# Performance work log

Hardware: AMD Instinct MI355X
Metric: run time of the kernel (lower is better)

Reference implementation:

```python
import jax, jax.numpy as jnp
import numpy as np

B, T, N, F = 64, 512, 14, 16
H_LSTM, H_GCN = 128, 64


def setup_inputs() -> dict:
    key = jax.random.key(0)
    ks = jax.random.split(key, 12)
    s = 0.05
    return {
        "x": jax.random.normal(ks[0], (B, T, N, F), dtype=jnp.float32),
        "adj": jax.random.uniform(ks[1], (N, N), dtype=jnp.float32),
        "W_ih": jax.random.normal(ks[2], (4 * H_LSTM, F), dtype=jnp.float32) * s,
        "W_hh": jax.random.normal(ks[3], (4 * H_LSTM, H_LSTM), dtype=jnp.float32) * s,
        "b_ih": jax.random.normal(ks[4], (4 * H_LSTM,), dtype=jnp.float32) * s,
        "b_hh": jax.random.normal(ks[5], (4 * H_LSTM,), dtype=jnp.float32) * s,
        "W_gcn": jax.random.normal(ks[6], (H_GCN, H_LSTM), dtype=jnp.float32) * s,
        "b_gcn": jax.random.normal(ks[7], (H_GCN,), dtype=jnp.float32) * s,
        "W_out": jax.random.normal(ks[8], (1, H_GCN), dtype=jnp.float32) * s,
        "b_out": jax.random.normal(ks[9], (1,), dtype=jnp.float32) * s,
        "W_lin1": jax.random.normal(ks[10], (28, N), dtype=jnp.float32) * s,
        "b_lin1": jax.random.normal(ks[11], (28,), dtype=jnp.float32) * s,
    }


def _lstm_last(x_seq, W_ih, W_hh, b_ih, b_hh):
    # x_seq: [M, T, F]; single-layer LSTM, torch gate order (i, f, g, o).
    M = x_seq.shape[0]
    H = W_hh.shape[1]
    # Precompute input contribution for all timesteps: [T, M, 4H]
    xw = jnp.einsum('mtf,gf->tmg', x_seq, W_ih) + b_ih + b_hh

    def step(carry, xt):
        h, c = carry
        gates = xt + h @ W_hh.T
        i, f, g, o = jnp.split(gates, 4, axis=-1)
        i = jax.nn.sigmoid(i)
        f = jax.nn.sigmoid(f)
        g = jnp.tanh(g)
        o = jax.nn.sigmoid(o)
        c = f * c + i * g
        h = o * jnp.tanh(c)
        return (h, c), None

    h0 = jnp.zeros((M, H), dtype=x_seq.dtype)
    (h_last, _), _ = jax.lax.scan(step, (h0, h0), xw)
    return h_last  # [M, H]


def reference(x, adj, W_ih, W_hh, b_ih, b_hh, W_gcn, b_gcn, W_out, b_out, W_lin1, b_lin1):
    Bb, Tt, Nn, Ff = x.shape
    # Batch all N node sequences into one recurrent pass (same math as per-node loop).
    x_nodes = x.transpose(0, 2, 1, 3).reshape(Bb * Nn, Tt, Ff)  # [B*N, T, F]
    h_last = _lstm_last(x_nodes, W_ih, W_hh, b_ih, b_hh)        # [B*N, H]
    lstm_out = h_last.reshape(Bb, Nn, -1)                        # [B, N, H]

    # Normalized adjacency with self-loops: D^-1/2 (A+I) D^-1/2
    A_hat = adj + jnp.eye(Nn, dtype=adj.dtype)
    d = A_hat.sum(axis=1) ** -0.5
    A_norm = d[:, None] * A_hat * d[None, :]

    x_gcn = jnp.einsum('ij,bjk->bik', A_norm, lstm_out)          # [B, N, H]
    x_gcn = jax.nn.relu(x_gcn @ W_gcn.T + b_gcn)                 # [B, N, H_GCN]
    x_gcn = (x_gcn @ W_out.T + b_out).squeeze(-1)                # [B, N]
    out = jax.nn.sigmoid(x_gcn @ W_lin1.T + b_lin1)              # [B, 28]
    return out
```

## Files before the change

kernel.cpp:

```cpp
#include <hip/hip_runtime.h>
#include <hip/hip_bf16.h>

#define B_   64
#define T_   512
#define N_   14
#define F_   16
#define H_   128
#define G4_  512
#define TCH  64
#define MBLK 4
#define NBLK 224

typedef __attribute__((ext_vector_type(8))) short bfrag;
typedef __attribute__((ext_vector_type(4))) float facc;
typedef __attribute__((ext_vector_type(4))) int   v4i;

#define L2E   1.4426950408889634f
#define L2E2  2.8853900817779268f

#define SX   0
#define SH   16384
#define LDSZ 17408

__device__ __forceinline__ short f2bf(float f) {
    unsigned u = __builtin_bit_cast(unsigned, f);
    return (short)((u + 0x7FFFu + ((u >> 16) & 1u)) >> 16);
}
__device__ __forceinline__ float bf2f(unsigned short s) {
    return __builtin_bit_cast(float, (unsigned)s << 16);
}
__device__ __forceinline__ unsigned cvt_pk_bf16(float a, float b) {
    unsigned r;
    asm("v_cvt_pk_bf16_f32 %0, %1, %2" : "=v"(r) : "v"(a), "v"(b));
    return r;
}
__device__ __forceinline__ v4i mfma_i8(v4i a, v4i b, v4i c) {
    v4i d;
    asm("v_mfma_i32_16x16x64_i8 %0, %1, %2, %3"
        : "=&v"(d) : "v"(a), "v"(b), "v"(c));
    return d;
}
__device__ __forceinline__ void bar() {
    asm volatile("s_waitcnt lgkmcnt(0)" ::: "memory");
    __builtin_amdgcn_s_barrier();
    asm volatile("" ::: "memory");
}

__global__ void prep1_kernel(const float* __restrict__ W_hh,
                             const float* __restrict__ b_ih, const float* __restrict__ b_hh,
                             float* __restrict__ inv127, float* __restrict__ sw,
                             float* __restrict__ bias) {
    const int g = threadIdx.x;
    float mx = 0.0f;
    for (int k = 0; k < H_; ++k) mx = fmaxf(mx, fabsf(W_hh[g * H_ + k]));
    const float sc = (g >= 256 && g < 384) ? L2E2 : L2E;
    inv127[g] = 127.0f / mx;
    sw[g]     = mx * sc * (1.0f / 16129.0f);
    bias[g]   = (b_ih[g] + b_hh[g]) * sc;
}

__global__ void prep2_kernel(const float* __restrict__ W_hh, const float* __restrict__ W_ih,
                             const float* __restrict__ inv127,
                             signed char* __restrict__ w8, short* __restrict__ wih_bf) {
    const int i = blockIdx.x * blockDim.x + threadIdx.x;
    if (i < G4_ * H_)
        w8[i] = (signed char)(int)rintf(W_hh[i] * inv127[i >> 7]);
    if (i < G4_ * 32) {
        const int n = i >> 5, k = i & 31;
        const float sc = (n >= 256 && n < 384) ? L2E2 : L2E;
        wih_bf[i] = (k < F_) ? f2bf(W_ih[n * F_ + k] * sc) : (short)0;
    }
}

template<int P, bool PREF>
__device__ __forceinline__ void lstm_step(char* lds, int tl,
    const v4i (&B8)[4][2], const bfrag (&Bx)[4], const facc (&bsp)[4],
    const float (&sw4)[4], facc (&xacc)[4], float& cc,
    int hrd, int xrd, int wboff)
{
    bar();
    const char* hb = lds + SH + P * 512;
    const v4i a0 = *(const v4i*)(hb + hrd);
    const v4i a1 = *(const v4i*)(hb + hrd + 256);

    const v4i z4 = (v4i){0, 0, 0, 0};
    v4i acc[4];
#pragma unroll
    for (int q = 0; q < 4; ++q) acc[q] = mfma_i8(a0, B8[q][0], z4);
#pragma unroll
    for (int q = 0; q < 4; ++q) acc[q] = mfma_i8(a1, B8[q][1], acc[q]);

    float z[4];
#pragma unroll
    for (int q = 0; q < 4; ++q)
        z[q] = (float)acc[q][0] * sw4[q] + xacc[q][0];

    const float ea = exp2f(-z[0]);
    const float ef = exp2f(-z[1]);
    const float eo = exp2f(-z[3]);
    const float eg = exp2f(-fabsf(z[2]));
    const float d1 = (1.0f + ea) * (1.0f + eg);
    const float d2 = 1.0f + ef;
    const float rP = __builtin_amdgcn_rcpf(d1 * d2);
    const float ig = __builtin_copysignf((1.0f - eg) * (rP * d2), z[2]);
    cc = (rP * d1) * cc + ig;
    const float ec = exp2f(-L2E2 * fabsf(cc));
    const float hv = __builtin_copysignf(
        (1.0f - ec) * __builtin_amdgcn_rcpf((1.0f + eo) * (1.0f + ec)), cc);
    *(signed char*)(lds + SH + (P ^ 1) * 512 + wboff) =
        (signed char)(int)rintf(hv * 127.0f);

    if (PREF) {
        const bfrag ax = *(const bfrag*)(lds + SX + (tl + 1) * 256 + xrd);
#pragma unroll
        for (int q = 0; q < 4; ++q)
            xacc[q] = __builtin_amdgcn_mfma_f32_16x16x32_bf16(ax, Bx[q], bsp[q], 0, 0, 0);
    }
}

__global__ __launch_bounds__(512, 2) void lstm_kernel(
    const float* __restrict__ x,
    const signed char* __restrict__ w8,
    const short* __restrict__ wih_bf,
    const float* __restrict__ bias,
    const float* __restrict__ sw,
    unsigned short* __restrict__ h_out)
{
    const int m0  = blockIdx.x * MBLK;
    const int tid = threadIdx.x;
    const int w   = tid >> 6, l = tid & 63;
    const int lr  = l & 15, lk = l >> 4;
    const int hcol = w * 16 + lr;

    __shared__ __align__(16) char lds[LDSZ];

    v4i   B8[4][2];
    bfrag Bx[4];
    facc  bsp[4];
    float sw4[4];
#pragma unroll
    for (int q = 0; q < 4; ++q) {
        const int n = q * H_ + hcol;
#pragma unroll
        for (int ks = 0; ks < 2; ++ks)
            B8[q][ks] = *(const v4i*)(w8 + n * 128 + ks * 64 + lk * 16);
        Bx[q] = *(const bfrag*)(wih_bf + n * 32 + lk * 8);
        const float b = bias[n];
        bsp[q] = (facc){b, b, b, b};
        sw4[q] = sw[n];
    }
#pragma unroll
    for (int q = 0; q < 4; ++q) {
        asm volatile("" : "+v"(B8[q][0]));
        asm volatile("" : "+v"(B8[q][1]));
        asm volatile("" : "+v"(Bx[q]));
        asm volatile("" : "+v"(bsp[q]));
    }

    const int hrd = lk * 64 + (lr >> 2) * 16;
    const int xrd = (lr >> 2) * 64 + lk * 16;
    const int wboff = w * 64 + lk * 16 + lr;

    const int skb = tid & 1, sseq = (tid >> 1) & 3, stl = tid >> 3;
    const int seqg = m0 + sseq;
    const int bb = seqg / N_, nn = seqg % N_;
    const float* xq = x + (((size_t)bb * T_ + stl) * N_ + nn) * F_ + skb * 8;
    const int sbyte = SX + stl * 256 + sseq * 64 + skb * 16;

    for (int i = tid; i < LDSZ / 4; i += 512) ((int*)lds)[i] = 0;
    float4 p0 = *(const float4*)xq, p1 = *(const float4*)(xq + 4);

    float cc = 0.0f;
    facc  xacc[4];
    bar();

#pragma unroll 1
    for (int chunk = 0; chunk < T_ / TCH; ++chunk) {
        {
            uint4 o;
            o.x = cvt_pk_bf16(p0.x, p0.y); o.y = cvt_pk_bf16(p0.z, p0.w);
            o.z = cvt_pk_bf16(p1.x, p1.y); o.w = cvt_pk_bf16(p1.z, p1.w);
            *(uint4*)(lds + sbyte) = o;
        }
        if (chunk + 1 < T_ / TCH) {
            xq += TCH * N_ * F_;
            p0 = *(const float4*)xq; p1 = *(const float4*)(xq + 4);
        }
        bar();

        {
            const bfrag ax = *(const bfrag*)(lds + SX + xrd);
#pragma unroll
            for (int q = 0; q < 4; ++q)
                xacc[q] = __builtin_amdgcn_mfma_f32_16x16x32_bf16(ax, Bx[q], bsp[q], 0, 0, 0);
        }

#pragma unroll 1
        for (int tl = 0; tl < TCH; tl += 2) {
            lstm_step<0, true>(lds, tl, B8, Bx, bsp, sw4, xacc, cc,
                               hrd, xrd, wboff);
            if (tl + 2 < TCH)
                lstm_step<1, true>(lds, tl + 1, B8, Bx, bsp, sw4, xacc, cc,
                                   hrd, xrd, wboff);
            else
                lstm_step<1, false>(lds, tl + 1, B8, Bx, bsp, sw4, xacc, cc,
                                    hrd, xrd, wboff);
        }
    }
    bar();

    {
        const int g = tid >> 7, c = tid & 127;
        const int addr = SH + (c >> 4) * 64 + g * 16 + (c & 15);
        const signed char v = *(const signed char*)(lds + addr);
        h_out[(size_t)(m0 + g) * H_ + c] = f2bf((float)v * (1.0f / 127.0f));
    }
}

__global__ __launch_bounds__(256) void head_kernel(
    const float* __restrict__ adj,
    const float* __restrict__ W_gcn, const float* __restrict__ b_gcn,
    const float* __restrict__ W_out, const float* __restrict__ b_out,
    const float* __restrict__ W_lin1, const float* __restrict__ b_lin1,
    const unsigned short* __restrict__ h_in,
    float* __restrict__ out)
{
    const int b   = blockIdx.x;
    const int tid = threadIdx.x;

    __shared__ float s_A[N_][N_];
    __shared__ float s_d[N_];
    __shared__ float s_h[N_][H_];
    __shared__ float s_xg[N_][H_];
    __shared__ float s_g1[N_][64];
    __shared__ float s_s[N_];

    for (int idx = tid; idx < N_ * H_; idx += 256)
        s_h[idx >> 7][idx & 127] = bf2f(h_in[(size_t)b * N_ * H_ + idx]);

    if (tid < N_) {
        float sum = 0.0f;
        for (int j = 0; j < N_; ++j)
            sum += adj[tid * N_ + j] + (tid == j ? 1.0f : 0.0f);
        s_d[tid] = rsqrtf(sum);
    }
    __syncthreads();

    if (tid < N_ * N_) {
        const int i = tid / N_, j = tid % N_;
        const float a = adj[i * N_ + j] + (i == j ? 1.0f : 0.0f);
        s_A[i][j] = s_d[i] * a * s_d[j];
    }
    __syncthreads();

    for (int idx = tid; idx < N_ * H_; idx += 256) {
        const int i = idx >> 7, k = idx & 127;
        float acc = 0.0f;
#pragma unroll
        for (int j = 0; j < N_; ++j) acc += s_A[i][j] * s_h[j][k];
        s_xg[i][k] = acc;
    }
    __syncthreads();

    for (int idx = tid; idx < N_ * 64; idx += 256) {
        const int i = idx >> 6, q = idx & 63;
        float a0 = 0.f, a1 = 0.f, a2 = 0.f, a3 = 0.f;
#pragma unroll
        for (int k = 0; k < H_; k += 4) {
            a0 += s_xg[i][k+0] * W_gcn[q * H_ + k+0];
            a1 += s_xg[i][k+1] * W_gcn[q * H_ + k+1];
            a2 += s_xg[i][k+2] * W_gcn[q * H_ + k+2];
            a3 += s_xg[i][k+3] * W_gcn[q * H_ + k+3];
        }
        const float acc = b_gcn[q] + ((a0 + a1) + (a2 + a3));
        s_g1[i][q] = fmaxf(acc, 0.0f);
    }
    __syncthreads();

    if (tid < N_) {
        float acc = b_out[0];
#pragma unroll
        for (int q = 0; q < 64; ++q) acc += s_g1[tid][q] * W_out[q];
        s_s[tid] = acc;
    }
    __syncthreads();

    if (tid < 28) {
        float acc = b_lin1[tid];
#pragma unroll
        for (int i = 0; i < N_; ++i) acc += s_s[i] * W_lin1[tid * N_ + i];
        out[b * 28 + tid] = 1.0f / (1.0f + __expf(-acc));
    }
}

extern "C" void kernel_launch(void* const* d_in, const int* in_sizes, int n_in,
                              void* d_out, int out_size, void* d_ws, size_t ws_size,
                              hipStream_t stream) {
    const float* x      = (const float*)d_in[0];
    const float* adj    = (const float*)d_in[1];
    const float* W_ih   = (const float*)d_in[2];
    const float* W_hh   = (const float*)d_in[3];
    const float* b_ih   = (const float*)d_in[4];
    const float* b_hh   = (const float*)d_in[5];
    const float* W_gcn  = (const float*)d_in[6];
    const float* b_gcn  = (const float*)d_in[7];
    const float* W_out  = (const float*)d_in[8];
    const float* b_out  = (const float*)d_in[9];
    const float* W_lin1 = (const float*)d_in[10];
    const float* b_lin1 = (const float*)d_in[11];
    float* out = (float*)d_out;

    char* ws = (char*)d_ws;
    signed char*    w8     = (signed char*)(ws);
    short*          wih_bf = (short*)(ws + 65536);
    float*          bias   = (float*)(ws + 98304);
    float*          sw     = (float*)(ws + 100352);
    float*          inv127 = (float*)(ws + 102400);
    unsigned short* h_last = (unsigned short*)(ws + 104448);

    prep1_kernel<<<1, 512, 0, stream>>>(W_hh, b_ih, b_hh, inv127, sw, bias);
    prep2_kernel<<<128, 512, 0, stream>>>(W_hh, W_ih, inv127, w8, wih_bf);
    lstm_kernel<<<NBLK, 512, 0, stream>>>(x, w8, wih_bf, bias, sw, h_last);
    head_kernel<<<B_, 256, 0, stream>>>(adj, W_gcn, b_gcn, W_out, b_out,
                                        W_lin1, b_lin1, h_last, out);
}
```

Measured before the change: 258.5 us.

## Halve sequences per LSTM block and use 4 waves each computing two hidden column tiles

Each LSTM block now handles 2 sequences instead of 4 and launches 448 blocks of 256 threads, so the work spreads across more CUs. Each wave covers 32 hidden columns using two MFMA column tiles, and each lane picks its own column's result (c1 select). Bias is now added in the scalar path instead of being folded into the MFMA accumulator. The cost is twice as many MFMAs per wave per step with half the useful rows, traded for more parallel blocks along the serial time recurrence.

```diff
diff --git a/kernel.cpp b/kernel.cpp
--- a/kernel.cpp
+++ b/kernel.cpp
@@ -8,8 +8,8 @@
 #define H_   128
 #define G4_  512
 #define TCH  64
-#define MBLK 4
-#define NBLK 224
+#define MBLK 2
+#define NBLK 448
 
 typedef __attribute__((ext_vector_type(8))) short bfrag;
 typedef __attribute__((ext_vector_type(4))) float facc;
@@ -19,8 +19,8 @@
 #define L2E2  2.8853900817779268f
 
 #define SX   0
-#define SH   16384
-#define LDSZ 17408
+#define SH   8192
+#define LDSZ 8704
 
 __device__ __forceinline__ short f2bf(float f) {
     unsigned u = __builtin_bit_cast(unsigned, f);
@@ -74,26 +74,36 @@
 
 template<int P, bool PREF>
 __device__ __forceinline__ void lstm_step(char* lds, int tl,
-    const v4i (&B8)[4][2], const bfrag (&Bx)[4], const facc (&bsp)[4],
-    const float (&sw4)[4], facc (&xacc)[4], float& cc,
-    int hrd, int xrd, int wboff)
+    const v4i (&B8)[4][2][2], const bfrag (&Bx)[4][2],
+    const float (&sw_own)[4], const float (&bias_own)[4],
+    facc (&xacc)[4][2], float& cc,
+    int hrd, int xrd, int wboff, bool c1)
 {
     bar();
-    const char* hb = lds + SH + P * 512;
+    const char* hb = lds + SH + P * 256;
     const v4i a0 = *(const v4i*)(hb + hrd);
-    const v4i a1 = *(const v4i*)(hb + hrd + 256);
+    const v4i a1 = *(const v4i*)(hb + hrd + 128);
 
     const v4i z4 = (v4i){0, 0, 0, 0};
-    v4i acc[4];
-#pragma unroll
-    for (int q = 0; q < 4; ++q) acc[q] = mfma_i8(a0, B8[q][0], z4);
-#pragma unroll
-    for (int q = 0; q < 4; ++q) acc[q] = mfma_i8(a1, B8[q][1], acc[q]);
+    v4i acc[4][2];
+#pragma unroll
+    for (int q = 0; q < 4; ++q)
+#pragma unroll
+        for (int c = 0; c < 2; ++c)
+            acc[q][c] = mfma_i8(a0, B8[q][0][c], z4);
+#pragma unroll
+    for (int q = 0; q < 4; ++q)
+#pragma unroll
+        for (int c = 0; c < 2; ++c)
+            acc[q][c] = mfma_i8(a1, B8[q][1][c], acc[q][c]);
 
     float z[4];
 #pragma unroll
-    for (int q = 0; q < 4; ++q)
-        z[q] = (float)acc[q][0] * sw4[q] + xacc[q][0];
+    for (int q = 0; q < 4; ++q) {
+        const int   ia = c1 ? acc[q][1][0] : acc[q][0][0];
+        const float xa = c1 ? xacc[q][1][0] : xacc[q][0][0];
+        z[q] = (float)ia * sw_own[q] + (xa + bias_own[q]);
+    }
 
     const float ea = exp2f(-z[0]);
     const float ef = exp2f(-z[1]);
@@ -107,18 +117,21 @@
     const float ec = exp2f(-L2E2 * fabsf(cc));
     const float hv = __builtin_copysignf(
         (1.0f - ec) * __builtin_amdgcn_rcpf((1.0f + eo) * (1.0f + ec)), cc);
-    *(signed char*)(lds + SH + (P ^ 1) * 512 + wboff) =
+    *(signed char*)(lds + SH + (P ^ 1) * 256 + wboff) =
         (signed char)(int)rintf(hv * 127.0f);
 
     if (PREF) {
-        const bfrag ax = *(const bfrag*)(lds + SX + (tl + 1) * 256 + xrd);
+        const bfrag ax = *(const bfrag*)(lds + SX + (tl + 1) * 128 + xrd);
+        const facc zf = (facc){0.f, 0.f, 0.f, 0.f};
 #pragma unroll
         for (int q = 0; q < 4; ++q)
-            xacc[q] = __builtin_amdgcn_mfma_f32_16x16x32_bf16(ax, Bx[q], bsp[q], 0, 0, 0);
-    }
-}
-
-__global__ __launch_bounds__(512, 2) void lstm_kernel(
+#pragma unroll
+            for (int c = 0; c < 2; ++c)
+                xacc[q][c] = __builtin_amdgcn_mfma_f32_16x16x32_bf16(ax, Bx[q][c], zf, 0, 0, 0);
+    }
+}
+
+__global__ __launch_bounds__(256, 2) void lstm_kernel(
     const float* __restrict__ x,
     const signed char* __restrict__ w8,
     const short* __restrict__ wih_bf,
@@ -130,48 +143,52 @@
     const int tid = threadIdx.x;
     const int w   = tid >> 6, l = tid & 63;
     const int lr  = l & 15, lk = l >> 4;
-    const int hcol = w * 16 + lr;
 
     __shared__ __align__(16) char lds[LDSZ];
 
-    v4i   B8[4][2];
-    bfrag Bx[4];
-    facc  bsp[4];
-    float sw4[4];
+    v4i   B8[4][2][2];
+    bfrag Bx[4][2];
+    float sw_own[4], bias_own[4];
+    const int owncol = 32 * w + 16 * (lk & 1) + lr;
 #pragma unroll
     for (int q = 0; q < 4; ++q) {
-        const int n = q * H_ + hcol;
-#pragma unroll
-        for (int ks = 0; ks < 2; ++ks)
-            B8[q][ks] = *(const v4i*)(w8 + n * 128 + ks * 64 + lk * 16);
-        Bx[q] = *(const bfrag*)(wih_bf + n * 32 + lk * 8);
-        const float b = bias[n];
-        bsp[q] = (facc){b, b, b, b};
-        sw4[q] = sw[n];
+#pragma unroll
+        for (int c = 0; c < 2; ++c) {
+            const int n = q * 128 + 32 * w + 16 * c + lr;
+#pragma unroll
+            for (int ks = 0; ks < 2; ++ks)
+                B8[q][ks][c] = *(const v4i*)(w8 + n * 128 + ks * 64 + lk * 16);
+            Bx[q][c] = *(const bfrag*)(wih_bf + n * 32 + lk * 8);
+        }
+        sw_own[q]   = sw[q * 128 + owncol];
+        bias_own[q] = bias[q * 128 + owncol];
     }
 #pragma unroll
     for (int q = 0; q < 4; ++q) {
-        asm volatile("" : "+v"(B8[q][0]));
-        asm volatile("" : "+v"(B8[q][1]));
-        asm volatile("" : "+v"(Bx[q]));
-        asm volatile("" : "+v"(bsp[q]));
-    }
-
-    const int hrd = lk * 64 + (lr >> 2) * 16;
-    const int xrd = (lr >> 2) * 64 + lk * 16;
-    const int wboff = w * 64 + lk * 16 + lr;
-
-    const int skb = tid & 1, sseq = (tid >> 1) & 3, stl = tid >> 3;
+#pragma unroll
+        for (int c = 0; c < 2; ++c) {
+            asm volatile("" : "+v"(B8[q][0][c]));
+            asm volatile("" : "+v"(B8[q][1][c]));
+            asm volatile("" : "+v"(Bx[q][c]));
+        }
+    }
+
+    const int hrd = lk * 32 + (lr >> 3) * 16;
+    const int xrd = (lr >> 3) * 64 + lk * 16;
+    const int wboff = (2 * w + (lk & 1)) * 32 + (lk >> 1) * 16 + lr;
+    const bool c1 = (lk & 1) != 0;
+
+    const int skb = tid & 1, sseq = (tid >> 1) & 1, stl = tid >> 2;
     const int seqg = m0 + sseq;
     const int bb = seqg / N_, nn = seqg % N_;
     const float* xq = x + (((size_t)bb * T_ + stl) * N_ + nn) * F_ + skb * 8;
-    const int sbyte = SX + stl * 256 + sseq * 64 + skb * 16;
-
-    for (int i = tid; i < LDSZ / 4; i += 512) ((int*)lds)[i] = 0;
+    const int sbyte = SX + stl * 128 + sseq * 64 + skb * 16;
+
+    for (int i = tid; i < LDSZ / 4; i += 256) ((int*)lds)[i] = 0;
     float4 p0 = *(const float4*)xq, p1 = *(const float4*)(xq + 4);
 
     float cc = 0.0f;
-    facc  xacc[4];
+    facc  xacc[4][2];
     bar();
 
 #pragma unroll 1
@@ -190,28 +207,31 @@
 
         {
             const bfrag ax = *(const bfrag*)(lds + SX + xrd);
+            const facc zf = (facc){0.f, 0.f, 0.f, 0.f};
 #pragma unroll
             for (int q = 0; q < 4; ++q)
-                xacc[q] = __builtin_amdgcn_mfma_f32_16x16x32_bf16(ax, Bx[q], bsp[q], 0, 0, 0);
+#pragma unroll
+                for (int c = 0; c < 2; ++c)
+                    xacc[q][c] = __builtin_amdgcn_mfma_f32_16x16x32_bf16(ax, Bx[q][c], zf, 0, 0, 0);
         }
 
 #pragma unroll 1
         for (int tl = 0; tl < TCH; tl += 2) {
-            lstm_step<0, true>(lds, tl, B8, Bx, bsp, sw4, xacc, cc,
-                               hrd, xrd, wboff);
+            lstm_step<0, true>(lds, tl, B8, Bx, sw_own, bias_own, xacc, cc,
+                               hrd, xrd, wboff, c1);
             if (tl + 2 < TCH)
-                lstm_step<1, true>(lds, tl + 1, B8, Bx, bsp, sw4, xacc, cc,
-                                   hrd, xrd, wboff);
+                lstm_step<1, true>(lds, tl + 1, B8, Bx, sw_own, bias_own, xacc, cc,
+                                   hrd, xrd, wboff, c1);
             else
-                lstm_step<1, false>(lds, tl + 1, B8, Bx, bsp, sw4, xacc, cc,
-                                    hrd, xrd, wboff);
+                lstm_step<1, false>(lds, tl + 1, B8, Bx, sw_own, bias_own, xacc, cc,
+                                    hrd, xrd, wboff, c1);
         }
     }
     bar();
 
     {
         const int g = tid >> 7, c = tid & 127;
-        const int addr = SH + (c >> 4) * 64 + g * 16 + (c & 15);
+        const int addr = SH + (c >> 4) * 32 + g * 16 + (c & 15);
         const signed char v = *(const signed char*)(lds + addr);
         h_out[(size_t)(m0 + g) * H_ + c] = f2bf((float)v * (1.0f / 127.0f));
     }
@@ -320,7 +340,7 @@
 
     prep1_kernel<<<1, 512, 0, stream>>>(W_hh, b_ih, b_hh, inv127, sw, bias);
     prep2_kernel<<<128, 512, 0, stream>>>(W_hh, W_ih, inv127, w8, wih_bf);
-    lstm_kernel<<<NBLK, 512, 0, stream>>>(x, w8, wih_bf, bias, sw, h_last);
+    lstm_kernel<<<NBLK, 256, 0, stream>>>(x, w8, wih_bf, bias, sw, h_last);
     head_kernel<<<B_, 256, 0, stream>>>(adj, W_gcn, b_gcn, W_out, b_out,
                                         W_lin1, b_lin1, h_last, out);
 }
```

Measured after the change: 340.7 us. 1.32x slower.
